# Performance work log

Hardware: AMD Instinct MI355X
Metric: run time of the kernel (lower is better)

Reference implementation:

```python
import jax, jax.numpy as jnp
import numpy as np

D = 512
H = 16
HD = D // H  # 32
S = 25
GRID = 5
DEPTH = 3
N_GENES = 250
EPS = 1e-5


def _rel_idx():
    # (dx, dy) offsets between all 25 grid positions, mapped to [0, 81)
    max_off = 2 * GRID - 1
    coords = np.stack(np.meshgrid(np.arange(GRID), np.arange(GRID), indexing='ij'))
    cf = coords.reshape(2, -1)  # [2, 25]
    rel = cf[:, :, None] - cf[:, None, :]  # [2, 25, 25]
    rel += GRID - 1
    return jnp.asarray(rel[0] * max_off + rel[1], dtype=jnp.int32)  # [25, 25]


def _layernorm(x, g, b):
    mu = jnp.mean(x, axis=-1, keepdims=True)
    var = jnp.mean(jnp.square(x - mu), axis=-1, keepdims=True)
    return (x - mu) * jax.lax.rsqrt(var + EPS) * g + b


def setup_inputs() -> dict:
    key = jax.random.key(0)
    ks = jax.random.split(key, 16)
    B = 4096
    f32 = jnp.float32
    inp = {
        'neighbor_feats': jax.random.normal(ks[0], (B, S, D), f32),
        'bias_table': jax.random.normal(ks[1], ((2 * GRID - 1) ** 2, H), f32) * 0.02,
        'ln1_g': jnp.ones((DEPTH, D), f32), 'ln1_b': jnp.zeros((DEPTH, D), f32),
        'wqkv': jax.random.normal(ks[2], (DEPTH, 3 * D, D), f32) * (1.0 / np.sqrt(D)),
        'bqkv': jnp.zeros((DEPTH, 3 * D), f32),
        'wo': jax.random.normal(ks[3], (DEPTH, D, D), f32) * (1.0 / np.sqrt(D)),
        'bo': jnp.zeros((DEPTH, D), f32),
        'ln2_g': jnp.ones((DEPTH, D), f32), 'ln2_b': jnp.zeros((DEPTH, D), f32),
        'w1': jax.random.normal(ks[4], (DEPTH, D, D), f32) * (1.0 / np.sqrt(D)),
        'b1': jnp.zeros((DEPTH, D), f32),
        'w2': jax.random.normal(ks[5], (DEPTH, D, D), f32) * (1.0 / np.sqrt(D)),
        'b2': jnp.zeros((DEPTH, D), f32),
        'lnf_g': jnp.ones((D,), f32), 'lnf_b': jnp.zeros((D,), f32),
        'pred_w': jax.random.normal(ks[6], (N_GENES, D), f32) * (1.0 / np.sqrt(D)),
        'pred_b': jnp.zeros((N_GENES,), f32),
    }
    return inp


def reference(neighbor_feats, bias_table, ln1_g, ln1_b, wqkv, bqkv, wo, bo,
              ln2_g, ln2_b, w1, b1, w2, b2, lnf_g, lnf_b, pred_w, pred_b):
    rel_idx = _rel_idx()
    # relative position bias: [H, 25, 25]
    attn_bias = bias_table[rel_idx].transpose(2, 0, 1)
    x = neighbor_feats
    scale = 1.0 / np.sqrt(HD)
    B = x.shape[0]
    for l in range(DEPTH):
        xn = _layernorm(x, ln1_g[l], ln1_b[l])
        qkv = xn @ wqkv[l].T + bqkv[l]  # [B, S, 3D]
        q, k, v = jnp.split(qkv, 3, axis=-1)
        q = q.reshape(B, S, H, HD).transpose(0, 2, 1, 3)
        k = k.reshape(B, S, H, HD).transpose(0, 2, 1, 3)
        v = v.reshape(B, S, H, HD).transpose(0, 2, 1, 3)
        scores = jnp.einsum('bhqd,bhkd->bhqk', q, k) * scale + attn_bias[None]
        attn = jax.nn.softmax(scores, axis=-1)
        o = jnp.einsum('bhqk,bhkd->bhqd', attn, v)  # [B, H, S, HD]
        o = o.transpose(0, 2, 1, 3).reshape(B, S, D)
        x = x + o @ wo[l].T + bo[l]
        h = _layernorm(x, ln2_g[l], ln2_b[l])
        h = jax.nn.gelu(h @ w1[l].T + b1[l], approximate=False)
        x = x + h @ w2[l].T + b2[l]
    x = _layernorm(x, lnf_g, lnf_b)
    pooled = jnp.mean(x, axis=1)
    pred = pooled @ pred_w.T + pred_b
    return (x, pred)
```

## Files before the change

kernel.cpp:

```cpp
#include <hip/hip_runtime.h>
#include <cstdint>
#include <cstddef>

#define D_ 512
#define S_ 25
#define H_ 16
#define HD_ 32
#define DEPTH_ 3
#define NG_ 250
#define BATCH_ 4096
#define M_ (BATCH_ * S_)
#define EPS_ 1e-5f

typedef __attribute__((ext_vector_type(8))) short short8;
typedef __attribute__((ext_vector_type(4))) short short4v;
typedef __attribute__((ext_vector_type(4))) float f32x4;

__device__ __forceinline__ float b2f(short s) {
  union { unsigned u; float f; } c;
  c.u = ((unsigned)(unsigned short)s) << 16;
  return c.f;
}
__device__ __forceinline__ short f2b(float f) {
  union { float f; unsigned u; } c; c.f = f;
  unsigned u = c.u + 0x7FFFu + ((c.u >> 16) & 1u);
  return (short)(u >> 16);
}

__device__ __forceinline__ void gld_lds16(const void* g, void* l) {
  __builtin_amdgcn_global_load_lds((const __attribute__((address_space(1))) void*)g,
                                   (__attribute__((address_space(3))) void*)l, 16, 0, 0);
}

__global__ __launch_bounds__(256) void cvt_f2b_ker(const float* __restrict__ in,
                                                   short* __restrict__ out, int n4) {
  int i = blockIdx.x * 256 + threadIdx.x;
  if (i < n4) {
    f32x4 v = *(const f32x4*)(in + (size_t)i * 4);
    short4v o;
#pragma unroll
    for (int j = 0; j < 4; ++j) o[j] = f2b(v[j]);
    *(short4v*)(out + (size_t)i * 4) = o;
  }
}

__global__ __launch_bounds__(256) void ln_to_bf16_ker(const float* __restrict__ x,
                                                      const float* __restrict__ g,
                                                      const float* __restrict__ bb,
                                                      short* __restrict__ out) {
  int row = (blockIdx.x << 2) + (threadIdx.x >> 6);
  int l = threadIdx.x & 63;
  const float* xr = x + (size_t)row * D_ + l * 8;
  f32x4 a = *(const f32x4*)xr;
  f32x4 b2v = *(const f32x4*)(xr + 4);
  float v[8];
#pragma unroll
  for (int j = 0; j < 4; ++j) { v[j] = a[j]; v[j + 4] = b2v[j]; }
  float s = 0.f, q = 0.f;
#pragma unroll
  for (int j = 0; j < 8; ++j) { s += v[j]; q += v[j] * v[j]; }
#pragma unroll
  for (int off = 32; off; off >>= 1) { s += __shfl_xor(s, off); q += __shfl_xor(q, off); }
  float mean = s * (1.0f / 512.0f);
  float var = q * (1.0f / 512.0f) - mean * mean;
  float rstd = rsqrtf(var + EPS_);
  const float* gp = g + l * 8;
  const float* bp = bb + l * 8;
  f32x4 g0 = *(const f32x4*)gp, g1 = *(const f32x4*)(gp + 4);
  f32x4 b0 = *(const f32x4*)bp, b1 = *(const f32x4*)(bp + 4);
  short8 o;
#pragma unroll
  for (int j = 0; j < 8; ++j) {
    float gg = (j < 4) ? g0[j] : g1[j - 4];
    float bv = (j < 4) ? b0[j] : b1[j - 4];
    o[j] = f2b((v[j] - mean) * rstd * gg + bv);
  }
  *(short8*)(out + (size_t)row * D_ + l * 8) = o;
}

__global__ __launch_bounds__(256) void ln_f32_inplace_ker(float* __restrict__ x,
                                                          const float* __restrict__ g,
                                                          const float* __restrict__ bb) {
  int row = (blockIdx.x << 2) + (threadIdx.x >> 6);
  int l = threadIdx.x & 63;
  float* xr = x + (size_t)row * D_ + l * 8;
  f32x4 a = *(const f32x4*)xr;
  f32x4 b2v = *(const f32x4*)(xr + 4);
  float v[8];
#pragma unroll
  for (int j = 0; j < 4; ++j) { v[j] = a[j]; v[j + 4] = b2v[j]; }
  float s = 0.f, q = 0.f;
#pragma unroll
  for (int j = 0; j < 8; ++j) { s += v[j]; q += v[j] * v[j]; }
#pragma unroll
  for (int off = 32; off; off >>= 1) { s += __shfl_xor(s, off); q += __shfl_xor(q, off); }
  float mean = s * (1.0f / 512.0f);
  float var = q * (1.0f / 512.0f) - mean * mean;
  float rstd = rsqrtf(var + EPS_);
  const float* gp = g + l * 8;
  const float* bp = bb + l * 8;
  f32x4 g0 = *(const f32x4*)gp, g1 = *(const f32x4*)(gp + 4);
  f32x4 b0 = *(const f32x4*)bp, b1 = *(const f32x4*)(bp + 4);
  f32x4 o0, o1;
#pragma unroll
  for (int j = 0; j < 4; ++j) {
    o0[j] = (v[j] - mean) * rstd * g0[j] + b0[j];
    o1[j] = (v[j + 4] - mean) * rstd * g1[j] + b1[j];
  }
  *(f32x4*)xr = o0;
  *(f32x4*)(xr + 4) = o1;
}

template <int EPI>
__global__ __launch_bounds__(256) void gemm_bf16_ker(const short* __restrict__ A,
                                                     const short* __restrict__ Bw,
                                                     const float* __restrict__ bias,
                                                     short* __restrict__ Obf,
                                                     float* __restrict__ Xres, int N) {
  constexpr int K = 512;
  __shared__ short At[128 * 64];
  __shared__ short Bt[128 * 64];
  const int tid = threadIdx.x;
  const int l = tid & 63;
  const int w = tid >> 6;
  const int wr = w >> 1, wc = w & 1;
  const int m0 = blockIdx.y * 128;
  const int n0 = blockIdx.x * 128;

  f32x4 acc[4][4] = {};

  for (int kt = 0; kt < K; kt += 64) {
#pragma unroll
    for (int i = 0; i < 4; ++i) {
      int chunk = i * 256 + tid;
      int row = chunk >> 3;
      int colS = ((chunk & 7) << 3) ^ ((row & 7) << 3);
      const short* ga = A + (size_t)(m0 + row) * K + kt + colS;
      const short* gb = Bw + (size_t)(n0 + row) * K + kt + colS;
      int base = (i * 256 + (w << 6)) << 3;
      gld_lds16(ga, &At[base]);
      gld_lds16(gb, &Bt[base]);
    }
    __syncthreads();
#pragma unroll
    for (int kk = 0; kk < 64; kk += 32) {
      short8 af[4], bfr[4];
#pragma unroll
      for (int mi = 0; mi < 4; ++mi) {
        int row = (wr << 6) + (mi << 4) + (l & 15);
        int colS = (kk + ((l >> 4) << 3)) ^ ((row & 7) << 3);
        af[mi] = *(const short8*)&At[row * 64 + colS];
      }
#pragma unroll
      for (int ni = 0; ni < 4; ++ni) {
        int row = (wc << 6) + (ni << 4) + (l & 15);
        int colS = (kk + ((l >> 4) << 3)) ^ ((row & 7) << 3);
        bfr[ni] = *(const short8*)&Bt[row * 64 + colS];
      }
#pragma unroll
      for (int mi = 0; mi < 4; ++mi)
#pragma unroll
        for (int ni = 0; ni < 4; ++ni)
          acc[mi][ni] = __builtin_amdgcn_mfma_f32_16x16x32_bf16(af[mi], bfr[ni], acc[mi][ni], 0, 0, 0);
    }
    __syncthreads();
  }

  const int lrow = (l >> 4) << 2;
  const int lcol = l & 15;
#pragma unroll
  for (int ni = 0; ni < 4; ++ni) {
    int gn = n0 + (wc << 6) + (ni << 4) + lcol;
    float bs = bias[gn];
#pragma unroll
    for (int mi = 0; mi < 4; ++mi) {
      int gm = m0 + (wr << 6) + (mi << 4) + lrow;
#pragma unroll
      for (int r = 0; r < 4; ++r) {
        float v = acc[mi][ni][r] + bs;
        size_t idx = (size_t)(gm + r) * N + gn;
        if (EPI == 0) {
          Obf[idx] = f2b(v);
        } else if (EPI == 1) {
          Xres[idx] += v;
        } else {
          Obf[idx] = f2b(0.5f * v * (1.0f + erff(v * 0.70710678118654752f)));
        }
      }
    }
  }
}

__global__ __launch_bounds__(512) void attn_ker(const short* __restrict__ qkv,
                                                const float* __restrict__ bias_table,
                                                short* __restrict__ o) {
  __shared__ short skv[S_ * 1024];
  int b = blockIdx.x;
  const short* cell = qkv + (size_t)b * S_ * 1536;
  for (int idx = threadIdx.x; idx < S_ * 1024 / 8; idx += 512) {
    int srow = idx >> 7;
    int c = (idx & 127) << 3;
    *(short8*)(skv + srow * 1024 + c) = *(const short8*)(cell + (size_t)srow * 1536 + 512 + c);
  }
  __syncthreads();
  int t = threadIdx.x;
  if (t < H_ * S_) {
    int h = t / S_;
    int i = t - h * S_;
    const short* qp = cell + (size_t)i * 1536 + h * HD_;
    float q[HD_];
#pragma unroll
    for (int c = 0; c < 4; ++c) {
      short8 v = *(const short8*)(qp + c * 8);
#pragma unroll
      for (int jj = 0; jj < 8; ++jj) q[c * 8 + jj] = b2f(v[jj]);
    }
    const float scale = 0.17677669529663687f;
    int xi = i / 5, yi = i - xi * 5;
    float sc[S_];
    float mx = -1e30f;
#pragma unroll
    for (int j = 0; j < S_; ++j) {
      const short* kp = skv + j * 1024 + h * HD_;
      float s = 0.f;
#pragma unroll
      for (int c = 0; c < 4; ++c) {
        short8 v = *(const short8*)(kp + c * 8);
#pragma unroll
        for (int jj = 0; jj < 8; ++jj) s += q[c * 8 + jj] * b2f(v[jj]);
      }
      int xj = j / 5, yj = j - xj * 5;
      int ridx = (xi - xj + 4) * 9 + (yi - yj + 4);
      s = s * scale + bias_table[ridx * H_ + h];
      sc[j] = s;
      mx = fmaxf(mx, s);
    }
    float den = 0.f;
#pragma unroll
    for (int j = 0; j < S_; ++j) {
      float e = __expf(sc[j] - mx);
      sc[j] = e;
      den += e;
    }
    float inv = 1.0f / den;
    float ov[HD_];
#pragma unroll
    for (int d = 0; d < HD_; ++d) ov[d] = 0.f;
#pragma unroll
    for (int j = 0; j < S_; ++j) {
      float pr = sc[j] * inv;
      const short* vp = skv + j * 1024 + 512 + h * HD_;
#pragma unroll
      for (int c = 0; c < 4; ++c) {
        short8 v = *(const short8*)(vp + c * 8);
#pragma unroll
        for (int jj = 0; jj < 8; ++jj) ov[c * 8 + jj] += pr * b2f(v[jj]);
      }
    }
    short* op = o + ((size_t)b * S_ + i) * D_ + h * HD_;
#pragma unroll
    for (int c = 0; c < 4; ++c) {
      short8 v;
#pragma unroll
      for (int jj = 0; jj < 8; ++jj) v[jj] = f2b(ov[c * 8 + jj]);
      *(short8*)(op + c * 8) = v;
    }
  }
}

__global__ __launch_bounds__(256) void pred_ker(const float* __restrict__ xf,
                                                const float* __restrict__ pw,
                                                const float* __restrict__ pb,
                                                float* __restrict__ pred) {
  __shared__ float pooled[D_];
  int b = blockIdx.x;
  const float* xb = xf + (size_t)b * S_ * D_;
  for (int d = threadIdx.x; d < D_; d += 256) {
    float s = 0.f;
#pragma unroll
    for (int j = 0; j < S_; ++j) s += xb[(size_t)j * D_ + d];
    pooled[d] = s * (1.0f / 25.0f);
  }
  __syncthreads();
  for (int n = threadIdx.x; n < NG_; n += 256) {
    const float* w = pw + (size_t)n * D_;
    float s = pb[n];
    for (int d = 0; d < D_; d += 4) {
      f32x4 wv = *(const f32x4*)(w + d);
      s += pooled[d] * wv[0] + pooled[d + 1] * wv[1] + pooled[d + 2] * wv[2] +
           pooled[d + 3] * wv[3];
    }
    pred[(size_t)b * NG_ + n] = s;
  }
}

extern "C" void kernel_launch(void* const* d_in, const int* in_sizes, int n_in,
                              void* d_out, int out_size, void* d_ws, size_t ws_size,
                              hipStream_t stream) {
  const float* nf = (const float*)d_in[0];
  const float* bias_table = (const float*)d_in[1];
  const float* ln1_g = (const float*)d_in[2];
  const float* ln1_b = (const float*)d_in[3];
  const float* wqkv = (const float*)d_in[4];
  const float* bqkv = (const float*)d_in[5];
  const float* wo = (const float*)d_in[6];
  const float* bo = (const float*)d_in[7];
  const float* ln2_g = (const float*)d_in[8];
  const float* ln2_b = (const float*)d_in[9];
  const float* w1 = (const float*)d_in[10];
  const float* b1 = (const float*)d_in[11];
  const float* w2 = (const float*)d_in[12];
  const float* b2 = (const float*)d_in[13];
  const float* lnf_g = (const float*)d_in[14];
  const float* lnf_b = (const float*)d_in[15];
  const float* pred_w = (const float*)d_in[16];
  const float* pred_b = (const float*)d_in[17];

  float* x = (float*)d_out;
  float* pred = x + (size_t)M_ * D_;

  char* p = (char*)d_ws;
  short* qkvb = (short*)p; p += (size_t)M_ * 1536 * 2;
  short* xnb = (short*)p;  p += (size_t)M_ * D_ * 2;
  short* ob = (short*)p;   p += (size_t)M_ * D_ * 2;
  short* hb = (short*)p;   p += (size_t)M_ * D_ * 2;
  short* wqkvb = (short*)p; p += (size_t)DEPTH_ * 1536 * 512 * 2;
  short* wob = (short*)p;   p += (size_t)DEPTH_ * 512 * 512 * 2;
  short* w1b = (short*)p;   p += (size_t)DEPTH_ * 512 * 512 * 2;
  short* w2b = (short*)p;   p += (size_t)DEPTH_ * 512 * 512 * 2;

  hipMemcpyAsync(x, nf, (size_t)M_ * D_ * sizeof(float), hipMemcpyDeviceToDevice, stream);

  {
    int n4 = DEPTH_ * 1536 * 512 / 4;
    cvt_f2b_ker<<<(n4 + 255) / 256, 256, 0, stream>>>(wqkv, wqkvb, n4);
    n4 = DEPTH_ * 512 * 512 / 4;
    cvt_f2b_ker<<<(n4 + 255) / 256, 256, 0, stream>>>(wo, wob, n4);
    cvt_f2b_ker<<<(n4 + 255) / 256, 256, 0, stream>>>(w1, w1b, n4);
    cvt_f2b_ker<<<(n4 + 255) / 256, 256, 0, stream>>>(w2, w2b, n4);
  }

  for (int L = 0; L < DEPTH_; ++L) {
    ln_to_bf16_ker<<<M_ / 4, 256, 0, stream>>>(x, ln1_g + L * D_, ln1_b + L * D_, xnb);
    gemm_bf16_ker<0><<<dim3(1536 / 128, M_ / 128), 256, 0, stream>>>(
        xnb, wqkvb + (size_t)L * 1536 * 512, bqkv + (size_t)L * 1536, qkvb, nullptr, 1536);
    attn_ker<<<BATCH_, 512, 0, stream>>>(qkvb, bias_table, ob);
    gemm_bf16_ker<1><<<dim3(512 / 128, M_ / 128), 256, 0, stream>>>(
        ob, wob + (size_t)L * 512 * 512, bo + (size_t)L * D_, nullptr, x, 512);
    ln_to_bf16_ker<<<M_ / 4, 256, 0, stream>>>(x, ln2_g + L * D_, ln2_b + L * D_, xnb);
    gemm_bf16_ker<2><<<dim3(512 / 128, M_ / 128), 256, 0, stream>>>(
        xnb, w1b + (size_t)L * 512 * 512, b1 + (size_t)L * D_, hb, nullptr, 512);
    gemm_bf16_ker<1><<<dim3(512 / 128, M_ / 128), 256, 0, stream>>>(
        hb, w2b + (size_t)L * 512 * 512, b2 + (size_t)L * D_, nullptr, x, 512);
  }

  ln_f32_inplace_ker<<<M_ / 4, 256, 0, stream>>>(x, lnf_g, lnf_b);
  pred_ker<<<BATCH_, 256, 0, stream>>>(x, pred_w, pred_b, pred);
}
```

Before: 4.729 ms.

## Swizzle GEMM blocks across XCDs, flatten attention threads, fuse initial residual copy

```diff
diff --git a/kernel.cpp b/kernel.cpp
--- a/kernel.cpp
+++ b/kernel.cpp
@@ -116,7 +116,9 @@
                                                      const short* __restrict__ Bw,
                                                      const float* __restrict__ bias,
                                                      short* __restrict__ Obf,
-                                                     float* __restrict__ Xres, int N) {
+                                                     float* __restrict__ Xres,
+                                                     const float* __restrict__ Xbase,
+                                                     int N, int nx) {
   constexpr int K = 512;
   __shared__ short At[128 * 64];
   __shared__ short Bt[128 * 64];
@@ -124,8 +126,13 @@
   const int l = tid & 63;
   const int w = tid >> 6;
   const int wr = w >> 1, wc = w & 1;
-  const int m0 = blockIdx.y * 128;
-  const int n0 = blockIdx.x * 128;
+  const int nwg = gridDim.x;
+  const int orig = blockIdx.x;
+  const int wg = ((orig & 7) * (nwg >> 3)) + (orig >> 3);
+  const int by = wg / nx;
+  const int bx = wg - by * nx;
+  const int m0 = by * 128;
+  const int n0 = bx * 128;
 
   f32x4 acc[4][4] = {};
 
@@ -183,88 +190,82 @@
           Obf[idx] = f2b(v);
         } else if (EPI == 1) {
           Xres[idx] += v;
+        } else if (EPI == 2) {
+          Obf[idx] = f2b(0.5f * v * (1.0f + erff(v * 0.70710678118654752f)));
         } else {
-          Obf[idx] = f2b(0.5f * v * (1.0f + erff(v * 0.70710678118654752f)));
+          Xres[idx] = Xbase[idx] + v;
         }
       }
     }
   }
 }
 
-__global__ __launch_bounds__(512) void attn_ker(const short* __restrict__ qkv,
+__global__ __launch_bounds__(256) void attn_ker(const short* __restrict__ qkv,
                                                 const float* __restrict__ bias_table,
                                                 short* __restrict__ o) {
-  __shared__ short skv[S_ * 1024];
-  int b = blockIdx.x;
+  unsigned p = blockIdx.x * 256 + threadIdx.x;
+  unsigned b = p / 400u;
+  unsigned r = p - b * 400u;
+  unsigned h = r / 25u;
+  unsigned i = r - h * 25u;
   const short* cell = qkv + (size_t)b * S_ * 1536;
-  for (int idx = threadIdx.x; idx < S_ * 1024 / 8; idx += 512) {
-    int srow = idx >> 7;
-    int c = (idx & 127) << 3;
-    *(short8*)(skv + srow * 1024 + c) = *(const short8*)(cell + (size_t)srow * 1536 + 512 + c);
-  }
-  __syncthreads();
-  int t = threadIdx.x;
-  if (t < H_ * S_) {
-    int h = t / S_;
-    int i = t - h * S_;
-    const short* qp = cell + (size_t)i * 1536 + h * HD_;
-    float q[HD_];
+  const short* qp = cell + (size_t)i * 1536 + h * HD_;
+  float q[HD_];
+#pragma unroll
+  for (int c = 0; c < 4; ++c) {
+    short8 v = *(const short8*)(qp + c * 8);
+#pragma unroll
+    for (int jj = 0; jj < 8; ++jj) q[c * 8 + jj] = b2f(v[jj]);
+  }
+  const float scale = 0.17677669529663687f;
+  int xi = i / 5, yi = i - xi * 5;
+  float sc[S_];
+  float mx = -1e30f;
+#pragma unroll
+  for (int j = 0; j < S_; ++j) {
+    const short* kp = cell + (size_t)j * 1536 + 512 + h * HD_;
+    float s = 0.f;
 #pragma unroll
     for (int c = 0; c < 4; ++c) {
-      short8 v = *(const short8*)(qp + c * 8);
-#pragma unroll
-      for (int jj = 0; jj < 8; ++jj) q[c * 8 + jj] = b2f(v[jj]);
-    }
-    const float scale = 0.17677669529663687f;
-    int xi = i / 5, yi = i - xi * 5;
-    float sc[S_];
-    float mx = -1e30f;
-#pragma unroll
-    for (int j = 0; j < S_; ++j) {
-      const short* kp = skv + j * 1024 + h * HD_;
-      float s = 0.f;
-#pragma unroll
-      for (int c = 0; c < 4; ++c) {
-        short8 v = *(const short8*)(kp + c * 8);
-#pragma unroll
-        for (int jj = 0; jj < 8; ++jj) s += q[c * 8 + jj] * b2f(v[jj]);
-      }
-      int xj = j / 5, yj = j - xj * 5;
-      int ridx = (xi - xj + 4) * 9 + (yi - yj + 4);
-      s = s * scale + bias_table[ridx * H_ + h];
-      sc[j] = s;
-      mx = fmaxf(mx, s);
-    }
-    float den = 0.f;
-#pragma unroll
-    for (int j = 0; j < S_; ++j) {
-      float e = __expf(sc[j] - mx);
-      sc[j] = e;
-      den += e;
-    }
-    float inv = 1.0f / den;
-    float ov[HD_];
-#pragma unroll
-    for (int d = 0; d < HD_; ++d) ov[d] = 0.f;
-#pragma unroll
-    for (int j = 0; j < S_; ++j) {
-      float pr = sc[j] * inv;
-      const short* vp = skv + j * 1024 + 512 + h * HD_;
-#pragma unroll
-      for (int c = 0; c < 4; ++c) {
-        short8 v = *(const short8*)(vp + c * 8);
-#pragma unroll
-        for (int jj = 0; jj < 8; ++jj) ov[c * 8 + jj] += pr * b2f(v[jj]);
-      }
-    }
-    short* op = o + ((size_t)b * S_ + i) * D_ + h * HD_;
+      short8 v = *(const short8*)(kp + c * 8);
+#pragma unroll
+      for (int jj = 0; jj < 8; ++jj) s += q[c * 8 + jj] * b2f(v[jj]);
+    }
+    int xj = j / 5, yj = j - xj * 5;
+    int ridx = (xi - xj + 4) * 9 + (yi - yj + 4);
+    s = s * scale + bias_table[ridx * H_ + h];
+    sc[j] = s;
+    mx = fmaxf(mx, s);
+  }
+  float den = 0.f;
+#pragma unroll
+  for (int j = 0; j < S_; ++j) {
+    float e = __expf(sc[j] - mx);
+    sc[j] = e;
+    den += e;
+  }
+  float inv = 1.0f / den;
+  float ov[HD_];
+#pragma unroll
+  for (int d = 0; d < HD_; ++d) ov[d] = 0.f;
+#pragma unroll
+  for (int j = 0; j < S_; ++j) {
+    float pr = sc[j] * inv;
+    const short* vp = cell + (size_t)j * 1536 + 1024 + h * HD_;
 #pragma unroll
     for (int c = 0; c < 4; ++c) {
-      short8 v;
-#pragma unroll
-      for (int jj = 0; jj < 8; ++jj) v[jj] = f2b(ov[c * 8 + jj]);
-      *(short8*)(op + c * 8) = v;
-    }
+      short8 v = *(const short8*)(vp + c * 8);
+#pragma unroll
+      for (int jj = 0; jj < 8; ++jj) ov[c * 8 + jj] += pr * b2f(v[jj]);
+    }
+  }
+  short* op = o + ((size_t)b * S_ + i) * D_ + h * HD_;
+#pragma unroll
+  for (int c = 0; c < 4; ++c) {
+    short8 v;
+#pragma unroll
+    for (int jj = 0; jj < 8; ++jj) v[jj] = f2b(ov[c * 8 + jj]);
+    *(short8*)(op + c * 8) = v;
   }
 }
 
@@ -329,8 +330,6 @@
   short* w1b = (short*)p;   p += (size_t)DEPTH_ * 512 * 512 * 2;
   short* w2b = (short*)p;   p += (size_t)DEPTH_ * 512 * 512 * 2;
 
-  hipMemcpyAsync(x, nf, (size_t)M_ * D_ * sizeof(float), hipMemcpyDeviceToDevice, stream);
-
   {
     int n4 = DEPTH_ * 1536 * 512 / 4;
     cvt_f2b_ker<<<(n4 + 255) / 256, 256, 0, stream>>>(wqkv, wqkvb, n4);
@@ -341,17 +340,24 @@
   }
 
   for (int L = 0; L < DEPTH_; ++L) {
-    ln_to_bf16_ker<<<M_ / 4, 256, 0, stream>>>(x, ln1_g + L * D_, ln1_b + L * D_, xnb);
-    gemm_bf16_ker<0><<<dim3(1536 / 128, M_ / 128), 256, 0, stream>>>(
-        xnb, wqkvb + (size_t)L * 1536 * 512, bqkv + (size_t)L * 1536, qkvb, nullptr, 1536);
-    attn_ker<<<BATCH_, 512, 0, stream>>>(qkvb, bias_table, ob);
-    gemm_bf16_ker<1><<<dim3(512 / 128, M_ / 128), 256, 0, stream>>>(
-        ob, wob + (size_t)L * 512 * 512, bo + (size_t)L * D_, nullptr, x, 512);
+    const float* xin = (L == 0) ? nf : x;
+    ln_to_bf16_ker<<<M_ / 4, 256, 0, stream>>>(xin, ln1_g + L * D_, ln1_b + L * D_, xnb);
+    gemm_bf16_ker<0><<<(1536 / 128) * (M_ / 128), 256, 0, stream>>>(
+        xnb, wqkvb + (size_t)L * 1536 * 512, bqkv + (size_t)L * 1536, qkvb, nullptr,
+        nullptr, 1536, 12);
+    attn_ker<<<BATCH_ * 400 / 256, 256, 0, stream>>>(qkvb, bias_table, ob);
+    if (L == 0) {
+      gemm_bf16_ker<3><<<(512 / 128) * (M_ / 128), 256, 0, stream>>>(
+          ob, wob, bo, nullptr, x, nf, 512, 4);
+    } else {
+      gemm_bf16_ker<1><<<(512 / 128) * (M_ / 128), 256, 0, stream>>>(
+          ob, wob + (size_t)L * 512 * 512, bo + (size_t)L * D_, nullptr, x, nullptr, 512, 4);
+    }
     ln_to_bf16_ker<<<M_ / 4, 256, 0, stream>>>(x, ln2_g + L * D_, ln2_b + L * D_, xnb);
-    gemm_bf16_ker<2><<<dim3(512 / 128, M_ / 128), 256, 0, stream>>>(
-        xnb, w1b + (size_t)L * 512 * 512, b1 + (size_t)L * D_, hb, nullptr, 512);
-    gemm_bf16_ker<1><<<dim3(512 / 128, M_ / 128), 256, 0, stream>>>(
-        hb, w2b + (size_t)L * 512 * 512, b2 + (size_t)L * D_, nullptr, x, 512);
+    gemm_bf16_ker<2><<<(512 / 128) * (M_ / 128), 256, 0, stream>>>(
+        xnb, w1b + (size_t)L * 512 * 512, b1 + (size_t)L * D_, hb, nullptr, nullptr, 512, 4);
+    gemm_bf16_ker<1><<<(512 / 128) * (M_ / 128), 256, 0, stream>>>(
+        hb, w2b + (size_t)L * 512 * 512, b2 + (size_t)L * D_, nullptr, x, nullptr, 512, 4);
   }
 
   ln_f32_inplace_ker<<<M_ / 4, 256, 0, stream>>>(x, lnf_g, lnf_b);
```

After: 5.839 ms. 23.5% more time.
